# Kernel tuning notes

Measured on AMD Instinct MI355X. Metric: run time of the kernel, lower is better.

The kernel has to match this reference:

```python
import jax, jax.numpy as jnp
import numpy as np

D = 2048      # input_dim
E = 64        # num_experts
TOPK = 8
N = 16384     # tokens


def setup_inputs() -> dict:
    key = jax.random.key(0)
    k_x, k_w1, k_b1, k_w2, k_b2 = jax.random.split(key, 5)
    s1 = 1.0 / np.sqrt(D)
    return {
        "x": jax.random.normal(k_x, (N, D), dtype=jnp.float32),
        "W1": jax.random.uniform(k_w1, (D, D), minval=-s1, maxval=s1, dtype=jnp.float32),
        "b1": jax.random.uniform(k_b1, (D,), minval=-s1, maxval=s1, dtype=jnp.float32),
        "W2": jax.random.uniform(k_w2, (D, E), minval=-s1, maxval=s1, dtype=jnp.float32),
        "b2": jax.random.uniform(k_b2, (E,), minval=-s1, maxval=s1, dtype=jnp.float32),
    }


def reference(x, W1, b1, W2, b2):
    # gate MLP: Linear -> GELU (exact, erf-based as torch nn.GELU default) -> Linear
    h = jax.nn.gelu(x @ W1 + b1, approximate=False)
    logits = h @ W2 + b2                              # [N, E]
    # eval mode: no noise added
    top_vals, top_idx = jax.lax.top_k(logits, TOPK)   # [N, K]
    top_w = jax.nn.softmax(top_vals, axis=-1)         # softmax over selected logits
    rows = jnp.arange(logits.shape[0])[:, None]       # [N, 1]
    routing_weights = jnp.zeros_like(logits).at[rows, top_idx].set(top_w)
    # load balance loss
    probs = jax.nn.softmax(logits, axis=-1)
    freq = (routing_weights > 0).astype(logits.dtype).mean(axis=0)   # [E]
    avg_prob = probs.mean(axis=0)                                    # [E]
    load_balance_loss = E * jnp.sum(freq * avg_prob)
    return routing_weights, top_idx, load_balance_loss
```

## Files before the change

kernel.cpp:

```cpp
#include <hip/hip_runtime.h>
#include <math.h>
#include <stdint.h>

#define N_TOK 16384
#define DIM   2048
#define NEXP  64
#define TOPK  8

#define BM 128
#define BN 128
#define BKE 32

typedef _Float16 half8  __attribute__((ext_vector_type(8)));
typedef float    f32x4  __attribute__((ext_vector_type(4)));

#define GLOBAL_AS __attribute__((address_space(1)))
#define LDS_AS    __attribute__((address_space(3)))

#define LO_SCALE     4096.0f
#define INV_LO_SCALE (1.0f / 4096.0f)

__device__ inline uint32_t pack_split(float v) {
    _Float16 hi = (_Float16)v;
    float r = (v - (float)hi) * LO_SCALE;
    _Float16 lo = (_Float16)r;
    return (uint32_t)__builtin_bit_cast(uint16_t, hi) |
           ((uint32_t)__builtin_bit_cast(uint16_t, lo) << 16);
}

__device__ inline _Float16 split_hi(float v) { return (_Float16)v; }
__device__ inline _Float16 split_lo(float v) {
    _Float16 hi = (_Float16)v;
    return (_Float16)((v - (float)hi) * LO_SCALE);
}

union U4H8 { uint32_t u[4]; half8 h; };

__device__ inline void load_frag(const uint32_t* base, int row, int quad,
                                 half8& hi, half8& lo) {
    const int sw = row & 7;
    const uint4 q0 = *(const uint4*)(base + row * 32 + (((quad * 2)     ^ sw) << 2));
    const uint4 q1 = *(const uint4*)(base + row * 32 + (((quad * 2 + 1) ^ sw) << 2));
    uint32_t u[8] = {q0.x, q0.y, q0.z, q0.w, q1.x, q1.y, q1.z, q1.w};
    U4H8 H, L;
    #pragma unroll
    for (int j = 0; j < 4; j++) {
        H.u[j] = (u[2 * j] & 0xffffu) | (u[2 * j + 1] << 16);
        L.u[j] = (u[2 * j] >> 16)     | (u[2 * j + 1] & 0xffff0000u);
    }
    hi = H.h; lo = L.h;
}

__device__ inline void load_frag2(const _Float16* base, int row, int quad,
                                  half8& hi, half8& lo) {
    const int sw = row & 7;
    hi = *(const half8*)(base + row * 64 + ((quad       ^ sw) << 3));
    lo = *(const half8*)(base + row * 64 + (((quad + 4) ^ sw) << 3));
}

#define CVT_XBLKS  ((N_TOK * DIM) / (256 * 8))
#define CVT_W1BLKS ((DIM / 32) * (DIM / 32))
#define CVT_W2BLKS ((NEXP * DIM) / 256)

__global__ __launch_bounds__(256) void convert_all(
    const float* __restrict__ x, const float* __restrict__ W1,
    const float* __restrict__ W2,
    _Float16* __restrict__ xhi, _Float16* __restrict__ xlo,
    _Float16* __restrict__ w1hi, _Float16* __restrict__ w1lo,
    uint32_t* __restrict__ W2Tp)
{
    const int b = blockIdx.x;
    if (b < CVT_XBLKS) {
        size_t i = ((size_t)b * 256 + threadIdx.x) * 8;
        float4 v0 = *(const float4*)(x + i);
        float4 v1 = *(const float4*)(x + i + 4);
        const float vv[8] = {v0.x, v0.y, v0.z, v0.w, v1.x, v1.y, v1.z, v1.w};
        half8 h, l;
        #pragma unroll
        for (int j = 0; j < 8; j++) { h[j] = split_hi(vv[j]); l[j] = split_lo(vv[j]); }
        *(half8*)(xhi + i) = h;
        *(half8*)(xlo + i) = l;
    } else if (b < CVT_XBLKS + CVT_W1BLKS) {
        __shared__ float s[32][33];
        const int bb = b - CVT_XBLKS;
        const int n0 = (bb & 63) * 32, k0 = (bb >> 6) * 32;
        const int tr = threadIdx.x & 31, tc = threadIdx.x >> 5;
        #pragma unroll
        for (int r = 0; r < 4; r++) {
            int row = tc + r * 8;
            s[row][tr] = W1[(size_t)(k0 + row) * DIM + n0 + tr];
        }
        __syncthreads();
        #pragma unroll
        for (int r = 0; r < 4; r++) {
            int row = tc + r * 8;
            float v = s[tr][row];
            w1hi[(size_t)(n0 + row) * DIM + k0 + tr] = split_hi(v);
            w1lo[(size_t)(n0 + row) * DIM + k0 + tr] = split_lo(v);
        }
    } else {
        const int i = (b - CVT_XBLKS - CVT_W1BLKS) * 256 + threadIdx.x;
        const int e = i >> 11, n = i & 2047;
        W2Tp[i] = pack_split(W2[(size_t)n * NEXP + e]);
    }
}

__global__ __launch_bounds__(256) void convert_x_inplace(float* __restrict__ x) {
    size_t i = ((size_t)blockIdx.x * 256 + threadIdx.x) * 4;
    float4 v = *(const float4*)(x + i);
    uint4 p;
    p.x = pack_split(v.x); p.y = pack_split(v.y);
    p.z = pack_split(v.z); p.w = pack_split(v.w);
    *(uint4*)(x + i) = p;
}

__global__ __launch_bounds__(256) void convert_w1t_packed(
    const float* __restrict__ W1, uint32_t* __restrict__ W1Tp)
{
    __shared__ float s[32][33];
    const int k0 = blockIdx.y * 32, n0 = blockIdx.x * 32;
    const int tr = threadIdx.x & 31, tc = threadIdx.x >> 5;
    #pragma unroll
    for (int r = 0; r < 4; r++) {
        int row = tc + r * 8;
        s[row][tr] = W1[(size_t)(k0 + row) * DIM + n0 + tr];
    }
    __syncthreads();
    #pragma unroll
    for (int r = 0; r < 4; r++) {
        int row = tc + r * 8;
        W1Tp[(size_t)(n0 + row) * DIM + k0 + tr] = pack_split(s[tr][row]);
    }
}

__global__ __launch_bounds__(256) void convert_w2t_packed(
    const float* __restrict__ W2, uint32_t* __restrict__ W2Tp) {
    int i = blockIdx.x * 256 + threadIdx.x;
    int e = i >> 11, n = i & 2047;
    W2Tp[i] = pack_split(W2[(size_t)n * NEXP + e]);
}


#define MFMA_F16(a_, b_, c_)  __builtin_amdgcn_mfma_f32_16x16x32_f16(a_, b_, c_, 0, 0, 0)

#define KSTEP(ASrc_, BSrc_, ASt_, BSt_, DOSTAGE_)                               \
    {                                                                           \
        if (DOSTAGE_) {                                                         \
            _Pragma("unroll")                                                   \
            for (int r = 0; r < 4; r++) {                                       \
                const int wslot = (r * 256 + wid * 64) << 2;                    \
                __builtin_amdgcn_global_load_lds(                               \
                    (const GLOBAL_AS uint32_t*)gA[r],                           \
                    (LDS_AS uint32_t*)((ASt_) + wslot), 16, 0, 0);              \
                __builtin_amdgcn_global_load_lds(                               \
                    (const GLOBAL_AS uint32_t*)gB[r],                           \
                    (LDS_AS uint32_t*)((BSt_) + wslot), 16, 0, 0);              \
                gA[r] += BKE; gB[r] += BKE;                                     \
            }                                                                   \
            asm volatile("s_waitcnt vmcnt(8)" ::: "memory");                    \
        } else {                                                                \
            asm volatile("s_waitcnt vmcnt(0)" ::: "memory");                    \
        }                                                                       \
        __builtin_amdgcn_s_barrier();                                           \
        half8 ah[4], al[4], bh[4], bl[4];                                       \
        _Pragma("unroll")                                                       \
        for (int mt = 0; mt < 4; mt++)                                          \
            load_frag2((const _Float16*)(ASrc_), wm + mt * 16 + l16, quad,      \
                       ah[mt], al[mt]);                                         \
        _Pragma("unroll")                                                       \
        for (int nt = 0; nt < 4; nt++)                                          \
            load_frag2((const _Float16*)(BSrc_), wn + nt * 16 + l16, quad,      \
                       bh[nt], bl[nt]);                                         \
        __builtin_amdgcn_s_setprio(1);                                          \
        _Pragma("unroll")                                                       \
        for (int mt = 0; mt < 4; mt++)                                          \
            _Pragma("unroll")                                                   \
            for (int nt = 0; nt < 4; nt++) {                                    \
                am[mt][nt] = MFMA_F16(ah[mt], bh[nt], am[mt][nt]);              \
                ac[mt][nt] = MFMA_F16(ah[mt], bl[nt], ac[mt][nt]);              \
                ac[mt][nt] = MFMA_F16(al[mt], bh[nt], ac[mt][nt]);              \
            }                                                                   \
        __builtin_amdgcn_s_setprio(0);                                          \
        asm volatile("s_waitcnt lgkmcnt(0)" ::: "memory");                      \
        __builtin_amdgcn_s_barrier();                                           \
    }

__global__ __launch_bounds__(256, 2) void gemm_fused_v2(
    const _Float16* __restrict__ xhi, const _Float16* __restrict__ xlo,
    const _Float16* __restrict__ w1hi, const _Float16* __restrict__ w1lo,
    const float* __restrict__ b1, const uint32_t* __restrict__ W2Tp,
    float* __restrict__ Lp)
{
    __shared__ uint32_t smem[16384];
    uint32_t* A0 = smem;
    uint32_t* B0 = smem + 4096;
    uint32_t* A1 = smem + 8192;
    uint32_t* B1 = smem + 12288;

    const int t    = threadIdx.x;
    const int wid  = t >> 6;
    const int lane = t & 63;
    const int quad = lane >> 4;
    const int l16  = lane & 15;

    const int lin = blockIdx.x;
    const int grp = lin >> 7;
    const int rem = lin & 127;
    const int m0 = (grp * 8 + (rem & 7)) * BM;
    const int n0 = (rem >> 3) * BN;

    const _Float16* gA[4];
    const _Float16* gB[4];
    #pragma unroll
    for (int r = 0; r < 4; r++) {
        int s_lin = r * 256 + t;
        int row = s_lin >> 3;
        int c   = (s_lin & 7) ^ (row & 7);
        gA[r] = (c < 4) ? xhi  + (size_t)(m0 + row) * DIM + c * 8
                        : xlo  + (size_t)(m0 + row) * DIM + (c - 4) * 8;
        gB[r] = (c < 4) ? w1hi + (size_t)(n0 + row) * DIM + c * 8
                        : w1lo + (size_t)(n0 + row) * DIM + (c - 4) * 8;
    }

    f32x4 am[4][4], ac[4][4];
    #pragma unroll
    for (int i = 0; i < 4; i++)
        #pragma unroll
        for (int j = 0; j < 4; j++) { am[i][j] = (f32x4)0.0f; ac[i][j] = (f32x4)0.0f; }

    const int wm = (wid & 1) * 64;
    const int wn = (wid >> 1) * 64;

    #pragma unroll
    for (int r = 0; r < 4; r++) {
        const int wslot = (r * 256 + wid * 64) << 2;
        __builtin_amdgcn_global_load_lds((const GLOBAL_AS uint32_t*)gA[r],
                                         (LDS_AS uint32_t*)(A0 + wslot), 16, 0, 0);
        __builtin_amdgcn_global_load_lds((const GLOBAL_AS uint32_t*)gB[r],
                                         (LDS_AS uint32_t*)(B0 + wslot), 16, 0, 0);
        gA[r] += BKE; gB[r] += BKE;
    }

    if ((lin >> 8) & 1) asm volatile("s_sleep 31");

    for (int kp = 0; kp < 32; kp++) {
        KSTEP(A0, B0, A1, B1, true);
        KSTEP(A1, B1, A0, B0, kp != 31);
    }

    uint32_t* Hs = smem;
    #pragma unroll
    for (int mt = 0; mt < 4; mt++)
        #pragma unroll
        for (int nt = 0; nt < 4; nt++) {
            const int coln = wn + nt * 16 + l16;
            const float b1v = b1[n0 + coln];
            #pragma unroll
            for (int r = 0; r < 4; r++) {
                float h = am[mt][nt][r] + ac[mt][nt][r] * INV_LO_SCALE + b1v;
                h = 0.5f * h * (1.0f + erff(h * 0.70710678118654752440f));
                const int rowm = wm + mt * 16 + quad * 4 + r;
                const int word = rowm * 128 + ((((coln >> 2) ^ (rowm & 7)) << 2) | (coln & 3));
                Hs[word] = pack_split(h);
            }
        }
    __syncthreads();

    f32x4 a2m[2][4], a2c[2][4];
    #pragma unroll
    for (int i = 0; i < 2; i++)
        #pragma unroll
        for (int j = 0; j < 4; j++) { a2m[i][j] = (f32x4)0.0f; a2c[i][j] = (f32x4)0.0f; }

    #pragma unroll
    for (int ks = 0; ks < 4; ks++) {
        half8 a2h[2], a2l[2];
        #pragma unroll
        for (int mt2 = 0; mt2 < 2; mt2++) {
            const int row = wid * 32 + mt2 * 16 + l16;
            const int sw  = row & 7;
            const int cb  = ks * 8 + quad * 2;
            const uint4 q0 = *(const uint4*)(Hs + row * 128 + ((cb ^ sw) << 2));
            const uint4 q1 = *(const uint4*)(Hs + row * 128 + (((cb + 1) ^ sw) << 2));
            uint32_t u[8] = {q0.x, q0.y, q0.z, q0.w, q1.x, q1.y, q1.z, q1.w};
            U4H8 H, L;
            #pragma unroll
            for (int j = 0; j < 4; j++) {
                H.u[j] = (u[2 * j] & 0xffffu) | (u[2 * j + 1] << 16);
                L.u[j] = (u[2 * j] >> 16)     | (u[2 * j + 1] & 0xffff0000u);
            }
            a2h[mt2] = H.h; a2l[mt2] = L.h;
        }
        #pragma unroll
        for (int et = 0; et < 4; et++) {
            const int e = et * 16 + l16;
            const uint32_t* wp = W2Tp + (size_t)e * DIM + n0 + ks * 32 + quad * 8;
            const uint4 q0 = *(const uint4*)wp;
            const uint4 q1 = *(const uint4*)(wp + 4);
            uint32_t u[8] = {q0.x, q0.y, q0.z, q0.w, q1.x, q1.y, q1.z, q1.w};
            U4H8 H, L;
            #pragma unroll
            for (int j = 0; j < 4; j++) {
                H.u[j] = (u[2 * j] & 0xffffu) | (u[2 * j + 1] << 16);
                L.u[j] = (u[2 * j] >> 16)     | (u[2 * j + 1] & 0xffff0000u);
            }
            #pragma unroll
            for (int mt2 = 0; mt2 < 2; mt2++) {
                a2m[mt2][et] = MFMA_F16(a2h[mt2], H.h, a2m[mt2][et]);
                a2c[mt2][et] = MFMA_F16(a2h[mt2], L.h, a2c[mt2][et]);
                a2c[mt2][et] = MFMA_F16(a2l[mt2], H.h, a2c[mt2][et]);
            }
        }
    }

    #pragma unroll
    for (int mt2 = 0; mt2 < 2; mt2++)
        #pragma unroll
        for (int et = 0; et < 4; et++)
            #pragma unroll
            for (int r = 0; r < 4; r++) {
                const float lg = a2m[mt2][et][r] + a2c[mt2][et][r] * INV_LO_SCALE;
                const int rowm = m0 + wid * 32 + mt2 * 16 + quad * 4 + r;
                const int e = et * 16 + l16;
                atomicAdd(&Lp[(size_t)rowm * NEXP + e], lg);
            }
}

__global__ __launch_bounds__(256, 2) void gemm_fused(
    const uint32_t* __restrict__ xp, const uint32_t* __restrict__ W1Tp,
    const float* __restrict__ b1, const uint32_t* __restrict__ W2Tp,
    float* __restrict__ Lp)
{
    __shared__ uint32_t smem[16384];
    uint32_t* Ap = smem;
    uint32_t* Bp = smem + 4096;

    const int t    = threadIdx.x;
    const int wid  = t >> 6;
    const int lane = t & 63;
    const int quad = lane >> 4;
    const int l16  = lane & 15;

    const int lin = blockIdx.x;
    const int grp = lin >> 7;
    const int rem = lin & 127;
    const int m0 = (grp * 8 + (rem & 7)) * BM;
    const int n0 = (rem >> 3) * BN;

    const uint32_t* gA[4];
    const uint32_t* gB[4];
    #pragma unroll
    for (int r = 0; r < 4; r++) {
        int s = r * 256 + t;
        int row = s >> 3;
        int c   = s & 7;
        int co  = (c ^ (row & 7)) << 2;
        gA[r] = xp   + (size_t)(m0 + row) * DIM + co;
        gB[r] = W1Tp + (size_t)(n0 + row) * DIM + co;
    }

    f32x4 am[4][4], ac[4][4];
    #pragma unroll
    for (int i = 0; i < 4; i++)
        #pragma unroll
        for (int j = 0; j < 4; j++) { am[i][j] = (f32x4)0.0f; ac[i][j] = (f32x4)0.0f; }

    const int wm = (wid & 1) * 64;
    const int wn = (wid >> 1) * 64;

    for (int k0 = 0; k0 < DIM; k0 += BKE) {
        #pragma unroll
        for (int r = 0; r < 4; r++) {
            const int wslot = (r * 256 + wid * 64) << 2;
            __builtin_amdgcn_global_load_lds((const GLOBAL_AS uint32_t*)gA[r],
                                             (LDS_AS uint32_t*)(Ap + wslot), 16, 0, 0);
            __builtin_amdgcn_global_load_lds((const GLOBAL_AS uint32_t*)gB[r],
                                             (LDS_AS uint32_t*)(Bp + wslot), 16, 0, 0);
            gA[r] += BKE; gB[r] += BKE;
        }
        __syncthreads();

        half8 ah[4], al[4], bh[4], bl[4];
        #pragma unroll
        for (int mt = 0; mt < 4; mt++)
            load_frag(Ap, wm + mt * 16 + l16, quad, ah[mt], al[mt]);
        #pragma unroll
        for (int nt = 0; nt < 4; nt++)
            load_frag(Bp, wn + nt * 16 + l16, quad, bh[nt], bl[nt]);

        #pragma unroll
        for (int mt = 0; mt < 4; mt++)
            #pragma unroll
            for (int nt = 0; nt < 4; nt++) {
                am[mt][nt] = MFMA_F16(ah[mt], bh[nt], am[mt][nt]);
                ac[mt][nt] = MFMA_F16(ah[mt], bl[nt], ac[mt][nt]);
                ac[mt][nt] = MFMA_F16(al[mt], bh[nt], ac[mt][nt]);
            }
        __syncthreads();
    }

    uint32_t* Hs = smem;
    #pragma unroll
    for (int mt = 0; mt < 4; mt++)
        #pragma unroll
        for (int nt = 0; nt < 4; nt++) {
            const int coln = wn + nt * 16 + l16;
            const float b1v = b1[n0 + coln];
            #pragma unroll
            for (int r = 0; r < 4; r++) {
                float h = am[mt][nt][r] + ac[mt][nt][r] * INV_LO_SCALE + b1v;
                h = 0.5f * h * (1.0f + erff(h * 0.70710678118654752440f));
                const int rowm = wm + mt * 16 + quad * 4 + r;
                const int word = rowm * 128 + ((((coln >> 2) ^ (rowm & 7)) << 2) | (coln & 3));
                Hs[word] = pack_split(h);
            }
        }
    __syncthreads();

    f32x4 a2m[2][4], a2c[2][4];
    #pragma unroll
    for (int i = 0; i < 2; i++)
        #pragma unroll
        for (int j = 0; j < 4; j++) { a2m[i][j] = (f32x4)0.0f; a2c[i][j] = (f32x4)0.0f; }

    #pragma unroll
    for (int ks = 0; ks < 4; ks++) {
        half8 a2h[2], a2l[2];
        #pragma unroll
        for (int mt2 = 0; mt2 < 2; mt2++) {
            const int row = wid * 32 + mt2 * 16 + l16;
            const int sw  = row & 7;
            const int cb  = ks * 8 + quad * 2;
            const uint4 q0 = *(const uint4*)(Hs + row * 128 + ((cb ^ sw) << 2));
            const uint4 q1 = *(const uint4*)(Hs + row * 128 + (((cb + 1) ^ sw) << 2));
            uint32_t u[8] = {q0.x, q0.y, q0.z, q0.w, q1.x, q1.y, q1.z, q1.w};
            U4H8 H, L;
            #pragma unroll
            for (int j = 0; j < 4; j++) {
                H.u[j] = (u[2 * j] & 0xffffu) | (u[2 * j + 1] << 16);
                L.u[j] = (u[2 * j] >> 16)     | (u[2 * j + 1] & 0xffff0000u);
            }
            a2h[mt2] = H.h; a2l[mt2] = L.h;
        }
        #pragma unroll
        for (int et = 0; et < 4; et++) {
            const int e = et * 16 + l16;
            const uint32_t* wp = W2Tp + (size_t)e * DIM + n0 + ks * 32 + quad * 8;
            const uint4 q0 = *(const uint4*)wp;
            const uint4 q1 = *(const uint4*)(wp + 4);
            uint32_t u[8] = {q0.x, q0.y, q0.z, q0.w, q1.x, q1.y, q1.z, q1.w};
            U4H8 H, L;
            #pragma unroll
            for (int j = 0; j < 4; j++) {
                H.u[j] = (u[2 * j] & 0xffffu) | (u[2 * j + 1] << 16);
                L.u[j] = (u[2 * j] >> 16)     | (u[2 * j + 1] & 0xffff0000u);
            }
            #pragma unroll
            for (int mt2 = 0; mt2 < 2; mt2++) {
                a2m[mt2][et] = MFMA_F16(a2h[mt2], H.h, a2m[mt2][et]);
                a2c[mt2][et] = MFMA_F16(a2h[mt2], L.h, a2c[mt2][et]);
                a2c[mt2][et] = MFMA_F16(a2l[mt2], H.h, a2c[mt2][et]);
            }
        }
    }

    #pragma unroll
    for (int mt2 = 0; mt2 < 2; mt2++)
        #pragma unroll
        for (int et = 0; et < 4; et++)
            #pragma unroll
            for (int r = 0; r < 4; r++) {
                const float lg = a2m[mt2][et][r] + a2c[mt2][et][r] * INV_LO_SCALE;
                const int rowm = m0 + wid * 32 + mt2 * 16 + quad * 4 + r;
                const int e = et * 16 + l16;
                atomicAdd(&Lp[(size_t)rowm * NEXP + e], lg);
            }
}

__global__ __launch_bounds__(256) void router_topk_v3(
    const float* __restrict__ Lp, const float* __restrict__ b2,
    float* __restrict__ out_rw, float* __restrict__ out_idx,
    float* __restrict__ gP, float* __restrict__ gI,
    float* __restrict__ out_loss, uint32_t* __restrict__ done)
{
    __shared__ float sP[NEXP];
    __shared__ float sI[NEXP];
    __shared__ uint32_t ticket;
    const int t = threadIdx.x;
    if (t < NEXP) { sP[t] = 0.f; sI[t] = 0.f; }
    __syncthreads();

    const int lane = t & 63;
    const int wv   = t >> 6;
    const float b2v = b2[lane];

    float accP = 0.f, accSel = 0.f;

    for (int i = 0; i < 16; i++) {
        const int tok = blockIdx.x * 64 + i * 4 + wv;
        float logit = Lp[(size_t)tok * NEXP + lane] + b2v;

        float mx = logit;
        #pragma unroll
        for (int off = 32; off >= 1; off >>= 1) mx = fmaxf(mx, __shfl_xor(mx, off));
        float p = expf(logit - mx);
        float ps = p;
        #pragma unroll
        for (int off = 32; off >= 1; off >>= 1) ps += __shfl_xor(ps, off);
        accP += p / ps;

        float cur = logit;
        float tv[TOPK]; int tix[TOPK];
        for (int k = 0; k < TOPK; k++) {
            float v = cur; int idx = lane;
            #pragma unroll
            for (int off = 32; off >= 1; off >>= 1) {
                float ov = __shfl_xor(v, off);
                int   oi = __shfl_xor(idx, off);
                if (ov > v || (ov == v && oi < idx)) { v = ov; idx = oi; }
            }
            tv[k] = v; tix[k] = idx;
            if (lane == idx) cur = -INFINITY;
        }

        float ev[TOPK], s = 0.f;
        #pragma unroll
        for (int k = 0; k < TOPK; k++) { ev[k] = expf(tv[k] - tv[0]); s += ev[k]; }
        float w = 0.f;
        #pragma unroll
        for (int k = 0; k < TOPK; k++)
            if (tix[k] == lane) { w = ev[k] / s; accSel += 1.f; }

        out_rw[(size_t)tok * NEXP + lane] = w;
        if (lane < TOPK) out_idx[(size_t)tok * TOPK + lane] = (float)tix[lane];
    }

    atomicAdd(&sP[lane], accP);
    atomicAdd(&sI[lane], accSel);
    __syncthreads();
    if (t < NEXP) { atomicAdd(&gP[t], sP[t]); atomicAdd(&gI[t], sI[t]); }

    __threadfence();
    if (t == 0) ticket = atomicAdd(done, 1u);
    __syncthreads();
    if (ticket == (uint32_t)(gridDim.x - 1)) {
        __threadfence();
        if (t < NEXP) {
            const float inv = 1.0f / (float)N_TOK;
            float fI = atomicAdd(&gI[t], 0.0f);
            float fP = atomicAdd(&gP[t], 0.0f);
            float v = (fI * inv) * (fP * inv);
            #pragma unroll
            for (int off = 32; off >= 1; off >>= 1) v += __shfl_xor(v, off);
            if (t == 0) out_loss[0] = (float)NEXP * v;
        }
    }
}

extern "C" void kernel_launch(void* const* d_in, const int* in_sizes, int n_in,
                              void* d_out, int out_size, void* d_ws, size_t ws_size,
                              hipStream_t stream) {
    const float* x  = (const float*)d_in[0];
    const float* W1 = (const float*)d_in[1];
    const float* b1 = (const float*)d_in[2];
    const float* W2 = (const float*)d_in[3];
    const float* b2 = (const float*)d_in[4];

    float* out_rw   = (float*)d_out;
    float* out_idx  = out_rw + (size_t)N_TOK * NEXP;
    float* out_loss = out_idx + (size_t)N_TOK * TOPK;

    const size_t SZ_X   = (size_t)N_TOK * DIM * 2;
    const size_t SZ_W1  = (size_t)DIM * DIM * 2;
    const size_t OFF_XHI   = 0;
    const size_t OFF_XLO   = OFF_XHI + SZ_X;
    const size_t OFF_W1HI  = OFF_XLO + SZ_X;
    const size_t OFF_W1LO  = OFF_W1HI + SZ_W1;
    const size_t OFF_W2T   = OFF_W1LO + SZ_W1;
    const size_t OFF_LP    = OFF_W2T + (size_t)DIM * NEXP * 4;
    const size_t OFF_G     = OFF_LP + (size_t)N_TOK * NEXP * 4;
    const size_t needed_v2 = OFF_G + 2 * NEXP * 4 + 16;

    const size_t P_W1T = 0;
    const size_t P_W2T = (size_t)16 << 20;
    const size_t P_LP  = (size_t)17 << 20;
    const size_t P_G   = P_LP + (size_t)N_TOK * NEXP * 4;
    const size_t needed_p = P_G + 2 * NEXP * 4 + 16;

    if (ws_size >= needed_v2) {
        _Float16* xhi  = (_Float16*)((char*)d_ws + OFF_XHI);
        _Float16* xlo  = (_Float16*)((char*)d_ws + OFF_XLO);
        _Float16* w1hi = (_Float16*)((char*)d_ws + OFF_W1HI);
        _Float16* w1lo = (_Float16*)((char*)d_ws + OFF_W1LO);
        uint32_t* W2Tp = (uint32_t*)((char*)d_ws + OFF_W2T);
        float* Lp = (float*)((char*)d_ws + OFF_LP);
        float* gP = (float*)((char*)d_ws + OFF_G);
        float* gI = gP + NEXP;
        uint32_t* done = (uint32_t*)(gI + NEXP);

        (void)hipMemsetAsync((char*)d_ws + OFF_LP, 0,
                             (size_t)N_TOK * NEXP * 4 + 2 * NEXP * 4 + 16, stream);
        convert_all<<<CVT_XBLKS + CVT_W1BLKS + CVT_W2BLKS, 256, 0, stream>>>(
            x, W1, W2, xhi, xlo, w1hi, w1lo, W2Tp);
        gemm_fused_v2<<<(N_TOK / BM) * (DIM / BN), 256, 0, stream>>>(
            xhi, xlo, w1hi, w1lo, b1, W2Tp, Lp);
        router_topk_v3<<<N_TOK / 64, 256, 0, stream>>>(
            Lp, b2, out_rw, out_idx, gP, gI, out_loss, done);
    } else if (ws_size >= needed_p) {
        uint32_t* W1Tp = (uint32_t*)((char*)d_ws + P_W1T);
        uint32_t* W2Tp = (uint32_t*)((char*)d_ws + P_W2T);
        float* Lp = (float*)((char*)d_ws + P_LP);
        float* gP = (float*)((char*)d_ws + P_G);
        float* gI = gP + NEXP;
        uint32_t* done = (uint32_t*)(gI + NEXP);

        (void)hipMemsetAsync((char*)d_ws + P_LP, 0,
                             (size_t)N_TOK * NEXP * 4 + 2 * NEXP * 4 + 16, stream);
        convert_x_inplace<<<(N_TOK * DIM) / (256 * 4), 256, 0, stream>>>((float*)d_in[0]);
        convert_w1t_packed<<<dim3(DIM / 32, DIM / 32), 256, 0, stream>>>(W1, W1Tp);
        convert_w2t_packed<<<(NEXP * DIM) / 256, 256, 0, stream>>>(W2, W2Tp);
        gemm_fused<<<(N_TOK / BM) * (DIM / BN), 256, 0, stream>>>(
            (const uint32_t*)d_in[0], W1Tp, b1, W2Tp, Lp);
        router_topk_v3<<<N_TOK / 64, 256, 0, stream>>>(
            Lp, b2, out_rw, out_idx, gP, gI, out_loss, done);
    }
}
```

Baseline: 742.7 us.

## Enlarge GEMM tile to 256 rows with eight waves and phased A-fragment MFMA

Doubles the M tile of the fused GEMM to 256 rows and launches 512-thread blocks with eight waves. Each wave now loads B fragments once per k-step and streams the A fragments one 16-row slice at a time, with barriers between the MFMA phases. The goal is to raise arithmetic intensity by reusing each W1 tile across more rows, and to lower register pressure by keeping only one A fragment live at a time. The staggered s_sleep is removed. The cost is double the LDS per block (128 KB), which likely limits the kernel to one block per CU, plus extra barriers per k-step.

```diff
diff --git a/kernel.cpp b/kernel.cpp
--- a/kernel.cpp
+++ b/kernel.cpp
@@ -7,7 +7,7 @@
 #define NEXP  64
 #define TOPK  8
 
-#define BM 128
+#define BM 256
 #define BN 128
 #define BKE 32
 
@@ -143,59 +143,70 @@
 
 #define MFMA_F16(a_, b_, c_)  __builtin_amdgcn_mfma_f32_16x16x32_f16(a_, b_, c_, 0, 0, 0)
 
-#define KSTEP(ASrc_, BSrc_, ASt_, BSt_, DOSTAGE_)                               \
+#define STAGE6(AT_, BT_)                                                        \
+    _Pragma("unroll")                                                           \
+    for (int r = 0; r < 4; r++) {                                               \
+        const int wslot = (r * 512 + wid * 64) << 2;                            \
+        __builtin_amdgcn_global_load_lds((const GLOBAL_AS uint32_t*)gA[r],      \
+            (LDS_AS uint32_t*)((AT_) + wslot), 16, 0, 0);                       \
+        gA[r] += BKE;                                                           \
+    }                                                                           \
+    _Pragma("unroll")                                                           \
+    for (int r = 0; r < 2; r++) {                                               \
+        const int wslot = (r * 512 + wid * 64) << 2;                            \
+        __builtin_amdgcn_global_load_lds((const GLOBAL_AS uint32_t*)gB[r],      \
+            (LDS_AS uint32_t*)((BT_) + wslot), 16, 0, 0);                       \
+        gB[r] += BKE;                                                           \
+    }
+
+#define PHASE_TAIL(mt_)                                                         \
+    __builtin_amdgcn_s_barrier();                                               \
+    asm volatile("s_waitcnt lgkmcnt(0)" ::: "memory");                          \
+    __builtin_amdgcn_s_setprio(1);                                              \
+    _Pragma("unroll")                                                           \
+    for (int nt = 0; nt < 4; nt++) {                                            \
+        am[mt_][nt] = MFMA_F16(ah, bh[nt], am[mt_][nt]);                        \
+        ac[mt_][nt] = MFMA_F16(ah, bl[nt], ac[mt_][nt]);                        \
+        ac[mt_][nt] = MFMA_F16(al, bh[nt], ac[mt_][nt]);                        \
+    }                                                                           \
+    __builtin_amdgcn_s_setprio(0);                                              \
+    __builtin_amdgcn_s_barrier();
+
+#define KSTEP(AS_, BS_, AT_, BT_, DOSTAGE_)                                     \
     {                                                                           \
         if (DOSTAGE_) {                                                         \
-            _Pragma("unroll")                                                   \
-            for (int r = 0; r < 4; r++) {                                       \
-                const int wslot = (r * 256 + wid * 64) << 2;                    \
-                __builtin_amdgcn_global_load_lds(                               \
-                    (const GLOBAL_AS uint32_t*)gA[r],                           \
-                    (LDS_AS uint32_t*)((ASt_) + wslot), 16, 0, 0);              \
-                __builtin_amdgcn_global_load_lds(                               \
-                    (const GLOBAL_AS uint32_t*)gB[r],                           \
-                    (LDS_AS uint32_t*)((BSt_) + wslot), 16, 0, 0);              \
-                gA[r] += BKE; gB[r] += BKE;                                     \
-            }                                                                   \
-            asm volatile("s_waitcnt vmcnt(8)" ::: "memory");                    \
+            STAGE6(AT_, BT_)                                                    \
+            asm volatile("s_waitcnt vmcnt(6)" ::: "memory");                    \
         } else {                                                                \
             asm volatile("s_waitcnt vmcnt(0)" ::: "memory");                    \
         }                                                                       \
         __builtin_amdgcn_s_barrier();                                           \
-        half8 ah[4], al[4], bh[4], bl[4];                                       \
-        _Pragma("unroll")                                                       \
-        for (int mt = 0; mt < 4; mt++)                                          \
-            load_frag2((const _Float16*)(ASrc_), wm + mt * 16 + l16, quad,      \
-                       ah[mt], al[mt]);                                         \
+        half8 bh[4], bl[4], ah, al;                                             \
         _Pragma("unroll")                                                       \
         for (int nt = 0; nt < 4; nt++)                                          \
-            load_frag2((const _Float16*)(BSrc_), wn + nt * 16 + l16, quad,      \
+            load_frag2((const _Float16*)(BS_), wn + nt * 16 + l16, quad,        \
                        bh[nt], bl[nt]);                                         \
-        __builtin_amdgcn_s_setprio(1);                                          \
-        _Pragma("unroll")                                                       \
-        for (int mt = 0; mt < 4; mt++)                                          \
-            _Pragma("unroll")                                                   \
-            for (int nt = 0; nt < 4; nt++) {                                    \
-                am[mt][nt] = MFMA_F16(ah[mt], bh[nt], am[mt][nt]);              \
-                ac[mt][nt] = MFMA_F16(ah[mt], bl[nt], ac[mt][nt]);              \
-                ac[mt][nt] = MFMA_F16(al[mt], bh[nt], ac[mt][nt]);              \
-            }                                                                   \
-        __builtin_amdgcn_s_setprio(0);                                          \
-        asm volatile("s_waitcnt lgkmcnt(0)" ::: "memory");                      \
-        __builtin_amdgcn_s_barrier();                                           \
-    }
-
-__global__ __launch_bounds__(256, 2) void gemm_fused_v2(
+        load_frag2((const _Float16*)(AS_), wm      + l16, quad, ah, al);        \
+        PHASE_TAIL(0)                                                           \
+        load_frag2((const _Float16*)(AS_), wm + 16 + l16, quad, ah, al);        \
+        PHASE_TAIL(1)                                                           \
+        load_frag2((const _Float16*)(AS_), wm + 32 + l16, quad, ah, al);        \
+        PHASE_TAIL(2)                                                           \
+        load_frag2((const _Float16*)(AS_), wm + 48 + l16, quad, ah, al);        \
+        PHASE_TAIL(3)                                                           \
+    }
+
+__global__ __launch_bounds__(512, 2) void gemm_fused_v2(
     const _Float16* __restrict__ xhi, const _Float16* __restrict__ xlo,
     const _Float16* __restrict__ w1hi, const _Float16* __restrict__ w1lo,
     const float* __restrict__ b1, const uint32_t* __restrict__ W2Tp,
     float* __restrict__ Lp)
 {
-    __shared__ uint32_t smem[16384];
+    __shared__ uint32_t smem[32768];
     uint32_t* A0 = smem;
-    uint32_t* B0 = smem + 4096;
-    uint32_t* A1 = smem + 8192;
-    uint32_t* B1 = smem + 12288;
+    uint32_t* B0 = smem + 8192;
+    uint32_t* A1 = smem + 12288;
+    uint32_t* B1 = smem + 20480;
 
     const int t    = threadIdx.x;
     const int wid  = t >> 6;
@@ -210,14 +221,20 @@
     const int n0 = (rem >> 3) * BN;
 
     const _Float16* gA[4];
-    const _Float16* gB[4];
+    const _Float16* gB[2];
     #pragma unroll
     for (int r = 0; r < 4; r++) {
-        int s_lin = r * 256 + t;
+        int s_lin = r * 512 + t;
         int row = s_lin >> 3;
         int c   = (s_lin & 7) ^ (row & 7);
-        gA[r] = (c < 4) ? xhi  + (size_t)(m0 + row) * DIM + c * 8
-                        : xlo  + (size_t)(m0 + row) * DIM + (c - 4) * 8;
+        gA[r] = (c < 4) ? xhi + (size_t)(m0 + row) * DIM + c * 8
+                        : xlo + (size_t)(m0 + row) * DIM + (c - 4) * 8;
+    }
+    #pragma unroll
+    for (int r = 0; r < 2; r++) {
+        int s_lin = r * 512 + t;
+        int row = s_lin >> 3;
+        int c   = (s_lin & 7) ^ (row & 7);
         gB[r] = (c < 4) ? w1hi + (size_t)(n0 + row) * DIM + c * 8
                         : w1lo + (size_t)(n0 + row) * DIM + (c - 4) * 8;
     }
@@ -228,20 +245,10 @@
         #pragma unroll
         for (int j = 0; j < 4; j++) { am[i][j] = (f32x4)0.0f; ac[i][j] = (f32x4)0.0f; }
 
-    const int wm = (wid & 1) * 64;
-    const int wn = (wid >> 1) * 64;
-
-    #pragma unroll
-    for (int r = 0; r < 4; r++) {
-        const int wslot = (r * 256 + wid * 64) << 2;
-        __builtin_amdgcn_global_load_lds((const GLOBAL_AS uint32_t*)gA[r],
-                                         (LDS_AS uint32_t*)(A0 + wslot), 16, 0, 0);
-        __builtin_amdgcn_global_load_lds((const GLOBAL_AS uint32_t*)gB[r],
-                                         (LDS_AS uint32_t*)(B0 + wslot), 16, 0, 0);
-        gA[r] += BKE; gB[r] += BKE;
-    }
-
-    if ((lin >> 8) & 1) asm volatile("s_sleep 31");
+    const int wm = (wid >> 1) * 64;
+    const int wn = (wid & 1) * 64;
+
+    STAGE6(A0, B0)
 
     for (int kp = 0; kp < 32; kp++) {
         KSTEP(A0, B0, A1, B1, true);
@@ -344,8 +351,8 @@
     const int lin = blockIdx.x;
     const int grp = lin >> 7;
     const int rem = lin & 127;
-    const int m0 = (grp * 8 + (rem & 7)) * BM;
-    const int n0 = (rem >> 3) * BN;
+    const int m0 = (grp * 8 + (rem & 7)) * 128;
+    const int n0 = (rem >> 3) * 128;
 
     const uint32_t* gA[4];
     const uint32_t* gB[4];
@@ -602,7 +609,7 @@
                              (size_t)N_TOK * NEXP * 4 + 2 * NEXP * 4 + 16, stream);
         convert_all<<<CVT_XBLKS + CVT_W1BLKS + CVT_W2BLKS, 256, 0, stream>>>(
             x, W1, W2, xhi, xlo, w1hi, w1lo, W2Tp);
-        gemm_fused_v2<<<(N_TOK / BM) * (DIM / BN), 256, 0, stream>>>(
+        gemm_fused_v2<<<(N_TOK / BM) * (DIM / BN), 512, 0, stream>>>(
             xhi, xlo, w1hi, w1lo, b1, W2Tp, Lp);
         router_topk_v3<<<N_TOK / 64, 256, 0, stream>>>(
             Lp, b2, out_rw, out_idx, gP, gI, out_loss, done);
@@ -619,7 +626,7 @@
         convert_x_inplace<<<(N_TOK * DIM) / (256 * 4), 256, 0, stream>>>((float*)d_in[0]);
         convert_w1t_packed<<<dim3(DIM / 32, DIM / 32), 256, 0, stream>>>(W1, W1Tp);
         convert_w2t_packed<<<(NEXP * DIM) / 256, 256, 0, stream>>>(W2, W2Tp);
-        gemm_fused<<<(N_TOK / BM) * (DIM / BN), 256, 0, stream>>>(
+        gemm_fused<<<(N_TOK / 128) * (DIM / 128), 256, 0, stream>>>(
             (const uint32_t*)d_in[0], W1Tp, b1, W2Tp, Lp);
         router_topk_v3<<<N_TOK / 64, 256, 0, stream>>>(
             Lp, b2, out_rw, out_idx, gP, gI, out_loss, done);
```

New measurement: 774.1 us. +4.2%, slower.
